# Optimization experiments

Hardware: AMD Instinct MI355X
Metric: run time of the kernel (lower is better)

## Reference

```python
import jax, jax.numpy as jnp
import numpy as np

TEMPERATURE = 0.1
NORM_EPS = 1e-12          # F.normalize default eps
SMALL_VAL = float(np.finfo(np.float32).tiny)  # pytorch-metric-learning small_val(float32)
NEG_INF = float(np.finfo(np.float32).min)     # c_f.neg_inf for masked logsumexp


def setup_inputs() -> dict:
    key = jax.random.key(0)
    k1, k2 = jax.random.split(key)
    N, D = 8192, 128
    emb = jax.random.normal(k1, (N, D), dtype=jnp.float32)
    labels = jax.random.randint(k2, (N,), 0, 1000, dtype=jnp.int64)
    return {"emb": emb, "labels": labels}


def reference(emb, labels):
    N = emb.shape[0]
    # F.normalize(emb, dim=1): x / max(||x||, eps)
    norms = jnp.linalg.norm(emb, axis=1, keepdims=True)
    x = emb / jnp.maximum(norms, NORM_EPS)

    # cosine similarity matrix [N, N], scaled by temperature
    mat = jnp.matmul(x, x.T) / TEMPERATURE

    same = labels[:, None] == labels[None, :]
    diag = jnp.eye(N, dtype=bool)
    pos_mask = same & ~diag          # same label, i != j
    keep_mask = ~diag                # pos + neg (all off-diagonal)

    # numerical stability: subtract detached row max (over full row, incl. diagonal)
    mat_max = jax.lax.stop_gradient(jnp.max(mat, axis=1, keepdims=True))
    mat = mat - mat_max

    # masked logsumexp over off-diagonal entries
    masked = jnp.where(keep_mask, mat, NEG_INF)
    denom = jax.nn.logsumexp(masked, axis=1, keepdims=True)  # [N, 1]

    log_prob = mat - denom
    pos_f = pos_mask.astype(mat.dtype)
    mean_log_prob_pos = jnp.sum(pos_f * log_prob, axis=1) / (
        jnp.sum(pos_f, axis=1) + SMALL_VAL
    )
    losses = -mean_log_prob_pos  # per-element losses
    # SumReducer: sum over elements
    return jnp.sum(losses)
```

## Files before the change

kernel.cpp:

```cpp
#include <hip/hip_runtime.h>
#include <hip/hip_bf16.h>


typedef __bf16 bf16_t;
typedef __bf16 bf16x2 __attribute__((ext_vector_type(2)));
typedef __bf16 bf16x8 __attribute__((ext_vector_type(8)));
typedef float f32x16 __attribute__((ext_vector_type(16)));

#define NN 8192
#define DIM 128
#define MAIN_BLOCKS 2080
#define SMALL_VAL 1.17549435e-38f
#define L2E10 14.4269504089f
#define LN2 0.69314718056f

__device__ inline size_t swz(int row, int lane) {
    int f = lane >> 3, hh = (lane >> 2) & 1, j = (lane & 3) << 1;
    return ((size_t)(row >> 5) * 4096) + f * 512 + hh * 256 + (row & 31) * 8 + j;
}

__global__ __launch_bounds__(256) void norm_csum(const float* __restrict__ emb,
                                                 const int* __restrict__ labels,
                                                 bf16_t* __restrict__ xsw,
                                                 float* __restrict__ cd_arr,
                                                 float* __restrict__ sd_arr,
                                                 float* __restrict__ cm1_arr,
                                                 float* __restrict__ se_acc,
                                                 float* __restrict__ out) {
    __shared__ float cs[DIM];
    __shared__ int rowlist[96];
    __shared__ int nrows;
    int cls = blockIdx.x;
    int wv = threadIdx.x >> 6, lane = threadIdx.x & 63;
    if (threadIdx.x < DIM) cs[threadIdx.x] = 0.f;
    if (threadIdx.x == 0) nrows = 0;
    if (threadIdx.x < 8) se_acc[cls * 8 + threadIdx.x] = 0.f;
    if (cls == 0 && threadIdx.x == 0) *out = 0.f;
    __syncthreads();

    float s0 = 0.f, s1 = 0.f;
    const int4* lab4 = (const int4*)(labels + wv * 2048);
#pragma unroll
    for (int it = 0; it < 8; ++it) {
        int4 l = lab4[it * 64 + lane];
        int base = wv * 2048 + it * 256;
#pragma unroll
        for (int cmp = 0; cmp < 4; ++cmp) {
            int li = (cmp == 0) ? l.x : (cmp == 1) ? l.y : (cmp == 2) ? l.z : l.w;
            unsigned long long m = __ballot(li == cls);
            while (m) {
                int bb = __builtin_ctzll(m);
                m &= m - 1;
                int row = base + 4 * bb + cmp;
                float2 v = ((const float2*)emb)[row * 64 + lane];
                float ss = fmaf(v.x, v.x, v.y * v.y);
#pragma unroll
                for (int mm = 1; mm < 64; mm <<= 1) ss += __shfl_xor(ss, mm, 64);
                float inv = 1.0f / fmaxf(sqrtf(ss), 1e-12f);
                bf16x2 o; o.x = (bf16_t)(v.x * inv); o.y = (bf16_t)(v.y * inv);
                *(bf16x2*)(xsw + swz(row, lane)) = o;
                s0 += (float)o.x; s1 += (float)o.y;
                if (lane == 0) {
                    int idx = atomicAdd(&nrows, 1);
                    if (idx < 96) rowlist[idx] = row;
                }
            }
        }
    }
    atomicAdd(&cs[2 * lane], s0);
    atomicAdd(&cs[2 * lane + 1], s1);
    __syncthreads();
    int n = nrows;
    for (int k = wv; k < n; k += 4) {
        int row = rowlist[k];
        bf16x2 xv = *(const bf16x2*)(xsw + swz(row, lane));
        float x0 = (float)xv.x, x1 = (float)xv.y;
        float cdp = fmaf(x0, cs[2 * lane], x1 * cs[2 * lane + 1]);
        float sdp = fmaf(x0, x0, x1 * x1);
#pragma unroll
        for (int mm = 1; mm < 64; mm <<= 1) {
            cdp += __shfl_xor(cdp, mm, 64);
            sdp += __shfl_xor(sdp, mm, 64);
        }
        if (lane == 0) {
            cd_arr[row] = cdp; sd_arr[row] = sdp; cm1_arr[row] = (float)(n - 1);
        }
    }
}

__global__ __launch_bounds__(256, 4) void supcon_main(const bf16_t* __restrict__ xsw,
                                                      float* __restrict__ se_acc) {
    __shared__ bf16_t bst[4 * 4096];
    __shared__ float cols[128];
    if (threadIdx.x < 128) cols[threadIdx.x] = 0.f;

    int b = blockIdx.x;
    int cq = (int)((sqrtf(8.f * (float)b + 1.f) - 1.f) * 0.5f);
    while ((cq + 1) * (cq + 2) / 2 <= b) ++cq;
    while (cq * (cq + 1) / 2 > b) --cq;
    int g = b - cq * (cq + 1) / 2;

    int wv = threadIdx.x >> 6, lane = threadIdx.x & 63;
    int I = 4 * g + wv;
    int c = lane & 31, h = lane >> 5;
    int laneoff = h * 256 + c * 8;

    const bf16_t* abase = xsw + (size_t)I * 4096 + laneoff;
    bf16x8 a[8];
#pragma unroll
    for (int f = 0; f < 8; ++f) a[f] = *(const bf16x8*)(abase + f * 512);

    {
        const uint4* gsrc = (const uint4*)(xsw + (size_t)cq * 4 * 4096);
        uint4* ldst = (uint4*)bst;
#pragma unroll
        for (int i = 0; i < 8; ++i)
            ldst[i * 256 + threadIdx.x] = gsrc[i * 256 + threadIdx.x];
    }
    __syncthreads();

    float se[16];
#pragma unroll
    for (int r = 0; r < 16; ++r) se[r] = 0.f;
    float colacc[4] = {0.f, 0.f, 0.f, 0.f};

#pragma unroll
    for (int t = 0; t < 4; ++t) {
        const bf16_t* bt = bst + t * 4096 + laneoff;
        bf16x8 bfr[8];
#pragma unroll
        for (int f = 0; f < 8; ++f) bfr[f] = *(const bf16x8*)(bt + f * 512);
        f32x16 acc;
#pragma unroll
        for (int r = 0; r < 16; ++r) acc[r] = 0.f;
#pragma unroll
        for (int f = 0; f < 8; ++f)
            acc = __builtin_amdgcn_mfma_f32_32x32x16_bf16(a[f], bfr[f], acc, 0, 0, 0);
        int ct = cq * 4 + t;
        if (ct >= I) {
            float c0 = 0.f, c1 = 0.f, c2 = 0.f, c3 = 0.f;
#pragma unroll
            for (int r = 0; r < 16; ++r) {
                float e = __builtin_amdgcn_exp2f(fmaf(acc[r], L2E10, -L2E10));
                se[r] += e;
                if ((r & 3) == 0) c0 += e; else if ((r & 3) == 1) c1 += e;
                else if ((r & 3) == 2) c2 += e; else c3 += e;
            }
            if (ct > I) colacc[t] = (c0 + c1) + (c2 + c3);
        }
    }

#pragma unroll
    for (int r = 0; r < 16; ++r) {
        float vv = se[r];
#pragma unroll
        for (int m = 1; m < 32; m <<= 1) vv += __shfl_xor(vv, m, 64);
        se[r] = vv;
    }
    if (c == 0) {
        int rowbase = I * 32 + 4 * h;
#pragma unroll
        for (int r = 0; r < 16; ++r)
            atomicAdd(&se_acc[rowbase + (r & 3) + 8 * (r >> 2)], se[r]);
    }

#pragma unroll
    for (int t = 0; t < 4; ++t) {
        float v = colacc[t] + __shfl_xor(colacc[t], 32, 64);
        if (h == 0) atomicAdd(&cols[t * 32 + c], v);
    }
    __syncthreads();
    if (threadIdx.x < 128)
        atomicAdd(&se_acc[cq * 128 + threadIdx.x], cols[threadIdx.x]);
}

__global__ __launch_bounds__(256) void finalize_kernel(const float* __restrict__ se_acc,
                                                       const float* __restrict__ cd_arr,
                                                       const float* __restrict__ sd_arr,
                                                       const float* __restrict__ cm1_arr,
                                                       float* __restrict__ out) {
    __shared__ float part[4];
    int i = blockIdx.x * 256 + threadIdx.x;
    float sd = sd_arr[i], cd = cd_arr[i], cm1 = cm1_arr[i];
    float diag = __builtin_amdgcn_exp2f(fmaf(sd, L2E10, -L2E10));
    float sev  = fmaxf(se_acc[i] - diag, 1e-30f);
    float lse  = fmaf(__builtin_amdgcn_logf(sev), LN2, 10.f);
    float loss = (cm1 * lse - 10.f * (cd - sd)) / (cm1 + SMALL_VAL);
#pragma unroll
    for (int m = 1; m < 64; m <<= 1) loss += __shfl_xor(loss, m, 64);
    int wv = threadIdx.x >> 6;
    if ((threadIdx.x & 63) == 0) part[wv] = loss;
    __syncthreads();
    if (threadIdx.x == 0) atomicAdd(out, part[0] + part[1] + part[2] + part[3]);
}

extern "C" void kernel_launch(void* const* d_in, const int* in_sizes, int n_in,
                              void* d_out, int out_size, void* d_ws, size_t ws_size,
                              hipStream_t stream) {
    const float* emb  = (const float*)d_in[0];
    const int* labels = (const int*)d_in[1];

    char* ws = (char*)d_ws;
    bf16_t* xsw = (bf16_t*)ws;
    float* se   = (float*)(ws + (size_t)NN * DIM * 2);
    float* cd   = se + NN;
    float* sd   = cd + NN;
    float* cm1  = sd + NN;

    norm_csum<<<1024, 256, 0, stream>>>(emb, labels, xsw, cd, sd, cm1, se, (float*)d_out);
    supcon_main<<<MAIN_BLOCKS, 256, 0, stream>>>(xsw, se);
    finalize_kernel<<<NN / 256, 256, 0, stream>>>(se, cd, sd, cm1, (float*)d_out);
}
```

Measured before the change: 99.11 us.

## Split prep into row-normalize and per-class blocks; fold finalize into main kernel

The prep kernel now launches 2048 extra blocks that normalize four rows each, writing the bf16 swizzled matrix and zeroing accumulators. The 1000 per-class blocks only handle their own class rows, computing self dot products and keeping normalized rows in LDS instead of re-reading global memory. The separate finalize kernel is removed: the last main block, found through an atomic counter with thread fences, computes and sums the per-row losses. This removes one launch and spreads the normalization across more blocks. In exchange, every class row is normalized twice, and the final reduction over all 8192 rows runs serially in a single block.

```diff
diff --git a/kernel.cpp b/kernel.cpp
--- a/kernel.cpp
+++ b/kernel.cpp
@@ -9,7 +9,7 @@
 
 #define NN 8192
 #define DIM 128
-#define MAIN_BLOCKS 2080
+#define NJOBS 2080
 #define SMALL_VAL 1.17549435e-38f
 #define L2E10 14.4269504089f
 #define LN2 0.69314718056f
@@ -19,25 +19,38 @@
     return ((size_t)(row >> 5) * 4096) + f * 512 + hh * 256 + (row & 31) * 8 + j;
 }
 
-__global__ __launch_bounds__(256) void norm_csum(const float* __restrict__ emb,
-                                                 const int* __restrict__ labels,
-                                                 bf16_t* __restrict__ xsw,
-                                                 float* __restrict__ cd_arr,
-                                                 float* __restrict__ sd_arr,
-                                                 float* __restrict__ cm1_arr,
-                                                 float* __restrict__ se_acc,
-                                                 float* __restrict__ out) {
+__global__ __launch_bounds__(256) void prep_kernel(const float* __restrict__ emb,
+                                                   const int* __restrict__ labels,
+                                                   bf16_t* __restrict__ xsw,
+                                                   float* __restrict__ cd_arr,
+                                                   float* __restrict__ sd_arr,
+                                                   float* __restrict__ cm1_arr,
+                                                   float* __restrict__ se_acc,
+                                                   int* __restrict__ done) {
+    __shared__ bf16x2 xloc[96][64];
     __shared__ float cs[DIM];
     __shared__ int rowlist[96];
     __shared__ int nrows;
-    int cls = blockIdx.x;
     int wv = threadIdx.x >> 6, lane = threadIdx.x & 63;
+
+    if (blockIdx.x < 2048) {
+        int row = blockIdx.x * 4 + wv;
+        float2 v = ((const float2*)emb)[row * 64 + lane];
+        float ss = fmaf(v.x, v.x, v.y * v.y);
+#pragma unroll
+        for (int m = 1; m < 64; m <<= 1) ss += __shfl_xor(ss, m, 64);
+        float inv = 1.0f / fmaxf(sqrtf(ss), 1e-12f);
+        bf16x2 o; o.x = (bf16_t)(v.x * inv); o.y = (bf16_t)(v.y * inv);
+        *(bf16x2*)(xsw + swz(row, lane)) = o;
+        if (threadIdx.x < 4) se_acc[blockIdx.x * 4 + threadIdx.x] = 0.f;
+        if (blockIdx.x == 0 && threadIdx.x == 0) *done = 0;
+        return;
+    }
+
+    int cls = blockIdx.x - 2048;
     if (threadIdx.x < DIM) cs[threadIdx.x] = 0.f;
     if (threadIdx.x == 0) nrows = 0;
-    if (threadIdx.x < 8) se_acc[cls * 8 + threadIdx.x] = 0.f;
-    if (cls == 0 && threadIdx.x == 0) *out = 0.f;
-    __syncthreads();
-
+    __syncthreads();
     float s0 = 0.f, s1 = 0.f;
     const int4* lab4 = (const int4*)(labels + wv * 2048);
 #pragma unroll
@@ -58,11 +71,18 @@
                 for (int mm = 1; mm < 64; mm <<= 1) ss += __shfl_xor(ss, mm, 64);
                 float inv = 1.0f / fmaxf(sqrtf(ss), 1e-12f);
                 bf16x2 o; o.x = (bf16_t)(v.x * inv); o.y = (bf16_t)(v.y * inv);
-                *(bf16x2*)(xsw + swz(row, lane)) = o;
-                s0 += (float)o.x; s1 += (float)o.y;
-                if (lane == 0) {
-                    int idx = atomicAdd(&nrows, 1);
-                    if (idx < 96) rowlist[idx] = row;
+                float x0 = (float)o.x, x1 = (float)o.y;
+                float sdp = fmaf(x0, x0, x1 * x1);
+#pragma unroll
+                for (int mm = 1; mm < 64; mm <<= 1) sdp += __shfl_xor(sdp, mm, 64);
+                s0 += x0; s1 += x1;
+                if (lane == 0) sd_arr[row] = sdp;
+                int idx = 0;
+                if (lane == 0) idx = atomicAdd(&nrows, 1);
+                idx = __shfl(idx, 0, 64);
+                if (idx < 96) {
+                    xloc[idx][lane] = o;
+                    if (lane == 0) rowlist[idx] = row;
                 }
             }
         }
@@ -71,27 +91,31 @@
     atomicAdd(&cs[2 * lane + 1], s1);
     __syncthreads();
     int n = nrows;
+    float cm1v = (float)(n - 1);
     for (int k = wv; k < n; k += 4) {
-        int row = rowlist[k];
-        bf16x2 xv = *(const bf16x2*)(xsw + swz(row, lane));
+        bf16x2 xv = xloc[k][lane];
         float x0 = (float)xv.x, x1 = (float)xv.y;
         float cdp = fmaf(x0, cs[2 * lane], x1 * cs[2 * lane + 1]);
-        float sdp = fmaf(x0, x0, x1 * x1);
-#pragma unroll
-        for (int mm = 1; mm < 64; mm <<= 1) {
-            cdp += __shfl_xor(cdp, mm, 64);
-            sdp += __shfl_xor(sdp, mm, 64);
+#pragma unroll
+        for (int mm = 1; mm < 64; mm <<= 1) cdp += __shfl_xor(cdp, mm, 64);
+        if (lane == 0) {
+            int row = rowlist[k];
+            cd_arr[row] = cdp;
+            cm1_arr[row] = cm1v;
         }
-        if (lane == 0) {
-            cd_arr[row] = cdp; sd_arr[row] = sdp; cm1_arr[row] = (float)(n - 1);
-        }
-    }
-}
-
-__global__ __launch_bounds__(256, 4) void supcon_main(const bf16_t* __restrict__ xsw,
-                                                      float* __restrict__ se_acc) {
+    }
+}
+
+__global__ __launch_bounds__(256, 4) void main_kernel(const bf16_t* __restrict__ xsw,
+                                                      const float* __restrict__ cd_arr,
+                                                      const float* __restrict__ sd_arr,
+                                                      const float* __restrict__ cm1_arr,
+                                                      float* __restrict__ se_acc,
+                                                      int* __restrict__ done,
+                                                      float* __restrict__ out) {
     __shared__ bf16_t bst[4 * 4096];
     __shared__ float cols[128];
+    __shared__ int amlast;
     if (threadIdx.x < 128) cols[threadIdx.x] = 0.f;
 
     int b = blockIdx.x;
@@ -172,26 +196,27 @@
     __syncthreads();
     if (threadIdx.x < 128)
         atomicAdd(&se_acc[cq * 128 + threadIdx.x], cols[threadIdx.x]);
-}
-
-__global__ __launch_bounds__(256) void finalize_kernel(const float* __restrict__ se_acc,
-                                                       const float* __restrict__ cd_arr,
-                                                       const float* __restrict__ sd_arr,
-                                                       const float* __restrict__ cm1_arr,
-                                                       float* __restrict__ out) {
-    __shared__ float part[4];
-    int i = blockIdx.x * 256 + threadIdx.x;
-    float sd = sd_arr[i], cd = cd_arr[i], cm1 = cm1_arr[i];
-    float diag = __builtin_amdgcn_exp2f(fmaf(sd, L2E10, -L2E10));
-    float sev  = fmaxf(se_acc[i] - diag, 1e-30f);
-    float lse  = fmaf(__builtin_amdgcn_logf(sev), LN2, 10.f);
-    float loss = (cm1 * lse - 10.f * (cd - sd)) / (cm1 + SMALL_VAL);
-#pragma unroll
-    for (int m = 1; m < 64; m <<= 1) loss += __shfl_xor(loss, m, 64);
-    int wv = threadIdx.x >> 6;
-    if ((threadIdx.x & 63) == 0) part[wv] = loss;
-    __syncthreads();
-    if (threadIdx.x == 0) atomicAdd(out, part[0] + part[1] + part[2] + part[3]);
+
+    __threadfence();
+    __syncthreads();
+    if (threadIdx.x == 0) amlast = (atomicAdd(done, 1) == NJOBS - 1);
+    __syncthreads();
+    if (!amlast) return;
+    __threadfence();
+
+    float lsum = 0.f;
+    for (int i = threadIdx.x; i < NN; i += 256) {
+        float sdv = sd_arr[i], cdv = cd_arr[i], cm1 = cm1_arr[i];
+        float diag = __builtin_amdgcn_exp2f(fmaf(sdv, L2E10, -L2E10));
+        float sev  = fmaxf(se_acc[i] - diag, 1e-30f);
+        float lse  = fmaf(__builtin_amdgcn_logf(sev), LN2, 10.f);
+        lsum += (cm1 * lse - 10.f * (cdv - sdv)) / (cm1 + SMALL_VAL);
+    }
+#pragma unroll
+    for (int m = 1; m < 64; m <<= 1) lsum += __shfl_xor(lsum, m, 64);
+    if (lane == 0) cols[wv] = lsum;
+    __syncthreads();
+    if (threadIdx.x == 0) *out = cols[0] + cols[1] + cols[2] + cols[3];
 }
 
 extern "C" void kernel_launch(void* const* d_in, const int* in_sizes, int n_in,
@@ -206,8 +231,8 @@
     float* cd   = se + NN;
     float* sd   = cd + NN;
     float* cm1  = sd + NN;
-
-    norm_csum<<<1024, 256, 0, stream>>>(emb, labels, xsw, cd, sd, cm1, se, (float*)d_out);
-    supcon_main<<<MAIN_BLOCKS, 256, 0, stream>>>(xsw, se);
-    finalize_kernel<<<NN / 256, 256, 0, stream>>>(se, cd, sd, cm1, (float*)d_out);
-}
+    int*   done = (int*)(cm1 + NN);
+
+    prep_kernel<<<2048 + 1000, 256, 0, stream>>>(emb, labels, xsw, cd, sd, cm1, se, done);
+    main_kernel<<<NJOBS, 256, 0, stream>>>(xsw, cd, sd, cm1, se, done, (float*)d_out);
+}
```

After: 218.5 us. 2.2x slower.

## Split each row-strip's upper-triangle tiles into per-wave segments without LDS staging

Applied to the files above, without the earlier changes.

Replaces the triangular block mapping, where each block staged four column tiles in LDS, with a per-wave decomposition. Each 32-row strip I is split into 32 segments over its remaining column tiles, and B fragments are loaded straight from global memory. Column sums are written to global memory with atomics on every tile instead of being reduced in shared memory first. The diagonal is now masked inside the diagonal tile rather than subtracted in finalize. The intent is better load balance and no block syncs, at the cost of more global loads and more global atomics.

```diff
diff --git a/kernel.cpp b/kernel.cpp
--- a/kernel.cpp
+++ b/kernel.cpp
@@ -9,7 +9,8 @@
 
 #define NN 8192
 #define DIM 128
-#define MAIN_BLOCKS 2080
+#define NB 256
+#define SEGS 32
 #define SMALL_VAL 1.17549435e-38f
 #define L2E10 14.4269504089f
 #define LN2 0.69314718056f
@@ -88,20 +89,15 @@
     }
 }
 
-__global__ __launch_bounds__(256, 4) void supcon_main(const bf16_t* __restrict__ xsw,
+__global__ __launch_bounds__(256, 4) void main_kernel(const bf16_t* __restrict__ xsw,
                                                       float* __restrict__ se_acc) {
-    __shared__ bf16_t bst[4 * 4096];
-    __shared__ float cols[128];
-    if (threadIdx.x < 128) cols[threadIdx.x] = 0.f;
+    int wid  = blockIdx.x * 4 + (threadIdx.x >> 6);
+    int lane = threadIdx.x & 63;
+    int I = wid >> 5, s = wid & 31;
+    int NT = NB - I;
+    int t0 = (NT * s) >> 5, t1 = (NT * (s + 1)) >> 5;
+    if (t0 == t1) return;
 
-    int b = blockIdx.x;
-    int cq = (int)((sqrtf(8.f * (float)b + 1.f) - 1.f) * 0.5f);
-    while ((cq + 1) * (cq + 2) / 2 <= b) ++cq;
-    while (cq * (cq + 1) / 2 > b) --cq;
-    int g = b - cq * (cq + 1) / 2;
-
-    int wv = threadIdx.x >> 6, lane = threadIdx.x & 63;
-    int I = 4 * g + wv;
     int c = lane & 31, h = lane >> 5;
     int laneoff = h * 256 + c * 8;
 
@@ -110,34 +106,32 @@
 #pragma unroll
     for (int f = 0; f < 8; ++f) a[f] = *(const bf16x8*)(abase + f * 512);
 
-    {
-        const uint4* gsrc = (const uint4*)(xsw + (size_t)cq * 4 * 4096);
-        uint4* ldst = (uint4*)bst;
-#pragma unroll
-        for (int i = 0; i < 8; ++i)
-            ldst[i * 256 + threadIdx.x] = gsrc[i * 256 + threadIdx.x];
-    }
-    __syncthreads();
-
     float se[16];
 #pragma unroll
     for (int r = 0; r < 16; ++r) se[r] = 0.f;
-    float colacc[4] = {0.f, 0.f, 0.f, 0.f};
 
+    for (int t = t0; t < t1; ++t) {
+        int J = I + t;
+        const bf16_t* bbase = xsw + (size_t)J * 4096 + laneoff;
+        bf16x8 b[8];
 #pragma unroll
-    for (int t = 0; t < 4; ++t) {
-        const bf16_t* bt = bst + t * 4096 + laneoff;
-        bf16x8 bfr[8];
-#pragma unroll
-        for (int f = 0; f < 8; ++f) bfr[f] = *(const bf16x8*)(bt + f * 512);
+        for (int f = 0; f < 8; ++f) b[f] = *(const bf16x8*)(bbase + f * 512);
         f32x16 acc;
 #pragma unroll
         for (int r = 0; r < 16; ++r) acc[r] = 0.f;
 #pragma unroll
         for (int f = 0; f < 8; ++f)
-            acc = __builtin_amdgcn_mfma_f32_32x32x16_bf16(a[f], bfr[f], acc, 0, 0, 0);
-        int ct = cq * 4 + t;
-        if (ct >= I) {
+            acc = __builtin_amdgcn_mfma_f32_32x32x16_bf16(a[f], b[f], acc, 0, 0, 0);
+
+        if (J == I) {
+#pragma unroll
+            for (int r = 0; r < 16; ++r) {
+                bool isdiag = c == ((r & 3) + 8 * (r >> 2) + 4 * h);
+                float e = isdiag ? 0.f
+                                 : __builtin_amdgcn_exp2f(fmaf(acc[r], L2E10, -L2E10));
+                se[r] += e;
+            }
+        } else {
             float c0 = 0.f, c1 = 0.f, c2 = 0.f, c3 = 0.f;
 #pragma unroll
             for (int r = 0; r < 16; ++r) {
@@ -146,7 +140,9 @@
                 if ((r & 3) == 0) c0 += e; else if ((r & 3) == 1) c1 += e;
                 else if ((r & 3) == 2) c2 += e; else c3 += e;
             }
-            if (ct > I) colacc[t] = (c0 + c1) + (c2 + c3);
+            float v = (c0 + c1) + (c2 + c3);
+            v += __shfl_xor(v, 32, 64);
+            if (h == 0) atomicAdd(&se_acc[J * 32 + c], v);
         }
     }
 
@@ -163,15 +159,6 @@
         for (int r = 0; r < 16; ++r)
             atomicAdd(&se_acc[rowbase + (r & 3) + 8 * (r >> 2)], se[r]);
     }
-
-#pragma unroll
-    for (int t = 0; t < 4; ++t) {
-        float v = colacc[t] + __shfl_xor(colacc[t], 32, 64);
-        if (h == 0) atomicAdd(&cols[t * 32 + c], v);
-    }
-    __syncthreads();
-    if (threadIdx.x < 128)
-        atomicAdd(&se_acc[cq * 128 + threadIdx.x], cols[threadIdx.x]);
 }
 
 __global__ __launch_bounds__(256) void finalize_kernel(const float* __restrict__ se_acc,
@@ -182,8 +169,7 @@
     __shared__ float part[4];
     int i = blockIdx.x * 256 + threadIdx.x;
     float sd = sd_arr[i], cd = cd_arr[i], cm1 = cm1_arr[i];
-    float diag = __builtin_amdgcn_exp2f(fmaf(sd, L2E10, -L2E10));
-    float sev  = fmaxf(se_acc[i] - diag, 1e-30f);
+    float sev  = fmaxf(se_acc[i], 1e-30f);
     float lse  = fmaf(__builtin_amdgcn_logf(sev), LN2, 10.f);
     float loss = (cm1 * lse - 10.f * (cd - sd)) / (cm1 + SMALL_VAL);
 #pragma unroll
@@ -208,6 +194,6 @@
     float* cm1  = sd + NN;
 
     norm_csum<<<1024, 256, 0, stream>>>(emb, labels, xsw, cd, sd, cm1, se, (float*)d_out);
-    supcon_main<<<MAIN_BLOCKS, 256, 0, stream>>>(xsw, se);
+    main_kernel<<<NB * SEGS / 4, 256, 0, stream>>>(xsw, se);
     finalize_kernel<<<NN / 256, 256, 0, stream>>>(se, cd, sd, cm1, (float*)d_out);
 }
```

New measurement: 103.2 us. +4.1%, slower.
